# Kernel tuning notes

Hardware: AMD Instinct MI355X
Metric: run time of the kernel (lower is better)

Reference implementation:

```python
import jax, jax.numpy as jnp
import numpy as np
from jax import lax

# ---- module hyperparams (from __init__ defaults) ----
REF_TR = 2.0
NUM_BANDS = 5
FREQ_LO, FREQ_HI = 0.008, 0.12

# ---- pywt.cwt('morl') internals, precision=10 ----
NPSI = 1024                                   # 2**10 samples of the wavelet
_x = np.linspace(-8.0, 8.0, NPSI)             # morlet support [-8, 8]
STEP = float(_x[1] - _x[0])
DOMAIN = 16.0                                 # x[-1] - x[0]
_psi = np.exp(-_x ** 2 / 2.0) * np.cos(5.0 * _x)   # 'morl' wavelet psi(t)
INT_PSI = jnp.asarray(np.cumsum(_psi) * STEP, dtype=jnp.float32)  # integrate_wavelet
LMAX = 544                                    # static bound: max scale ~33.4 -> L <= 535


def _cwt_band(gpad, scale):
    """pywt conv-method CWT at one scale for all regions.
    gpad: [R, N+1+2*LMAX] = first difference of zero-extended signal, zero-padded.
    Uses identity: diff(convolve(x, K[::-1])) == correlate(diff-ext(x), K) shifted.
    """
    R = gpad.shape[0]
    N = gpad.shape[1] - 1 - 2 * LMAX
    i = jnp.arange(LMAX)
    # len(np.arange(scale*16 + 1)) for non-integer scale*16
    L0 = jnp.floor(scale * DOMAIN).astype(jnp.int32) + 2
    j = jnp.floor(i.astype(jnp.float32) / (scale * STEP)).astype(jnp.int32)
    mask = (i < L0) & (j < NPSI)              # pywt filters j < int_psi.size
    K = jnp.where(mask, INT_PSI[jnp.clip(j, 0, NPSI - 1)], 0.0)  # int_psi_scale (unreversed)
    L = mask.sum()                            # effective kernel length (mask is a prefix)
    # cross-correlation of gpad with K (lax.conv does correlation, no kernel flip)
    corr = lax.conv_general_dilated(gpad[:, None, :], K[None, None, :], (1,), 'VALID',
                                    dimension_numbers=('NCH', 'OIH', 'NCH'))[:, 0, :]
    # center crop: coef[t] = -sqrt(s) * (c[t+f+1]-c[t+f]),  f = floor((L-2)/2)
    start = LMAX + (L - 2) // 2 + 2 - L
    coef = lax.dynamic_slice(corr, (jnp.int32(0), start), (R, N))
    return jnp.abs(-jnp.sqrt(scale) * coef)


def _forward(timeseries, tr_values, log_scale_params, bandwidth_params):
    B, R, N = timeseries.shape
    tr_factors = tr_values / REF_TR
    scales = jnp.exp(log_scale_params)[None, :] / tr_factors[:, None]      # [B, bands]
    # frequency bands [B, bands, 2]
    center = 1.0 / (scales * tr_values[:, None])
    bw = bandwidth_params[None, :]
    low = jnp.maximum(FREQ_LO, center * (1.0 - bw / 2.0))
    high = jnp.minimum(FREQ_HI, center * (1.0 + bw / 2.0))
    frequency_bands = jnp.stack([low, high], axis=-1)
    # first difference of zero-extended signal: g[m] = x[m] - x[m-1], x=0 outside [0,N)
    g = jnp.diff(jnp.pad(timeseries, ((0, 0), (0, 0), (1, 1))), axis=-1)    # [B,R,N+1]
    gpad = jnp.pad(g, ((0, 0), (0, 0), (LMAX, LMAX)))
    per_sample = jax.vmap(_cwt_band, in_axes=(None, 0))                     # over bands
    coeffs = jax.vmap(per_sample, in_axes=(0, 0))(gpad, scales)             # [B,bands,R,N]
    coeffs = jnp.transpose(coeffs, (0, 2, 1, 3))                            # [B,R,bands,N]
    return coeffs, frequency_bands


def setup_inputs() -> dict:
    key = jax.random.key(0)
    k1, k2 = jax.random.split(key)
    B, R, T = 8, 400, 1200
    timeseries = jax.random.normal(k1, (B, R, T), dtype=jnp.float32)
    # realistic fMRI TRs in [1.5, 2.5] s (keeps adaptive scales <= 33.4 < LMAX/16)
    tr_values = 1.5 + jax.random.uniform(k2, (B,), dtype=jnp.float32)
    log_scale_params = jnp.linspace(np.log(5.0), np.log(25.0), NUM_BANDS).astype(jnp.float32)
    bandwidth_params = 0.1 * jnp.ones((NUM_BANDS,), dtype=jnp.float32)
    return {"timeseries": timeseries, "tr_values": tr_values,
            "log_scale_params": log_scale_params, "bandwidth_params": bandwidth_params}


def reference(timeseries, tr_values, log_scale_params, bandwidth_params):
    return _forward(timeseries, tr_values, log_scale_params, bandwidth_params)
```

## Files before the change

### kernel.cpp

```cpp
#include <hip/hip_runtime.h>
#include <math.h>

#define B_    8
#define R_    400
#define N_    1200
#define S_    5
#define LMAX_ 544
#define NPSI_ 1024
#define KPAD  560
#define WINMAX 1760
#define T_    20

#define WS_K      0
#define WS_SCALE  (40*KPAD)
#define WS_SQS    (WS_SCALE + 40)
#define WS_L      (WS_SQS + 40)
#define WS_START  (WS_L + 40)

__device__ __forceinline__ float4 lds_ld4(const float* base, int dw) {
    int g = dw >> 2;
    g ^= (g >> 3) & 7;
    return *(const float4*)(base + (g << 2));
}

__global__ __launch_bounds__(256) void setup_kernel(
    const float* __restrict__ tr,
    const float* __restrict__ lsp,
    const float* __restrict__ bwp,
    float* __restrict__ ws,
    float* __restrict__ out_bands)
{
    __shared__ double psi_sh[NPSI_];
    __shared__ float  intpsi[NPSI_];
    __shared__ double wtot[4];
    __shared__ float  scale_sh[40];
    __shared__ int    cnt_sh[40];
    const double STEP_D = 16.0 / 1023.0;
    const float  STEP_F = (float)(16.0 / 1023.0);
    const int tid = threadIdx.x;

    if (tid < 40) cnt_sh[tid] = 0;

    for (int k = tid; k < NPSI_; k += 256) {
        double x = (k == NPSI_ - 1) ? 8.0 : (-8.0 + (double)k * STEP_D);
        psi_sh[k] = exp(-x * x * 0.5) * cos(5.0 * x);
    }
    __syncthreads();

    {
        double a0 = psi_sh[4 * tid + 0], a1 = psi_sh[4 * tid + 1];
        double a2 = psi_sh[4 * tid + 2], a3 = psi_sh[4 * tid + 3];
        double s1 = a0 + a1, s2 = s1 + a2, s3 = s2 + a3;
        double run = s3;
        #pragma unroll
        for (int d = 1; d < 64; d <<= 1) {
            double o = __shfl_up(run, (unsigned)d, 64);
            if ((tid & 63) >= d) run += o;
        }
        if ((tid & 63) == 63) wtot[tid >> 6] = run;
        __syncthreads();
        double woff = 0.0;
        const int w = tid >> 6;
        #pragma unroll
        for (int k = 0; k < 4; ++k) if (k < w) woff += wtot[k];
        double excl = woff + run - s3;
        intpsi[4 * tid + 0] = (float)((excl + a0) * STEP_D);
        intpsi[4 * tid + 1] = (float)((excl + s1) * STEP_D);
        intpsi[4 * tid + 2] = (float)((excl + s2) * STEP_D);
        intpsi[4 * tid + 3] = (float)((excl + s3) * STEP_D);
    }

    if (tid < 40) {
        int b = tid / S_, s = tid % S_;
        float trf   = tr[b] / 2.0f;
        float scale = expf(lsp[s]) / trf;
        scale_sh[tid] = scale;
        ws[WS_SCALE + tid] = scale;
        ws[WS_SQS + tid]   = sqrtf(scale);
        float center = 1.0f / (scale * tr[b]);
        float bw = bwp[s];
        out_bands[2 * tid + 0] = fmaxf(0.008f, center * (1.0f - bw * 0.5f));
        out_bands[2 * tid + 1] = fminf(0.12f,  center * (1.0f + bw * 0.5f));
    }
    __syncthreads();

    {
        const int wv = tid >> 6, ln = tid & 63;
        for (int c = wv; c < 40 * 9; c += 4) {
            int p = c / 9, i = (c % 9) * 64 + ln;
            float scale = scale_sh[p];
            float sst   = scale * STEP_F;
            int   L0    = (int)floorf(scale * 16.0f) + 2;
            bool m = false;
            if (i < LMAX_) {
                int j = (int)floorf((float)i / sst);
                m = (i < L0) && (j < NPSI_);
            }
            unsigned long long bal = __ballot(m);
            if (ln == 0) atomicAdd(&cnt_sh[p], __popcll(bal));
        }
    }
    __syncthreads();
    if (tid < 40) {
        int L = cnt_sh[tid];
        ((int*)(ws + WS_L))[tid]     = L;
        ((int*)(ws + WS_START))[tid] = LMAX_ + (L - 2) / 2 + 2 - L;
    }

    for (int idx = tid; idx < 40 * KPAD; idx += 256) {
        int p = idx / KPAD, i = idx % KPAD;
        float v = 0.0f;
        if (i < LMAX_) {
            float scale = scale_sh[p];
            float sst   = scale * STEP_F;
            int   L0    = (int)floorf(scale * 16.0f) + 2;
            int   j     = (int)floorf((float)i / sst);
            if (i < L0 && j < NPSI_) {
                int jc = j < 0 ? 0 : (j > NPSI_ - 1 ? NPSI_ - 1 : j);
                v = intpsi[jc];
            }
        }
        ws[WS_K + idx] = v;
    }
}

__global__ __launch_bounds__(256) void cwt_main_kernel(
    const float* __restrict__ ts,
    const float* __restrict__ ws,
    float* __restrict__ out)
{
    const float* Kbase     = ws + WS_K;
    const float* sqs_arr   = ws + WS_SQS;
    const int*   L_arr     = (const int*)(ws + WS_L);
    const int*   start_arr = (const int*)(ws + WS_START);

    const int bid = blockIdx.x;
    const int rg  = bid % 100;
    const int b   = (bid / 100) % B_;
    const int s   = 4 - (bid / (100 * B_));
    const int pair = b * S_ + s;

    const int   L      = L_arr[pair];
    const int   start  = start_arr[pair];
    const float sqs    = sqs_arr[pair];
    const int   wstart = start - LMAX_;
    const int   Lpad   = ((L + 23) / 24) * 24;

    __shared__ __align__(16) float gwin[4 * WINMAX];

    const int tid = threadIdx.x;

    for (int wv = 0; wv < 4; ++wv) {
        const int r = rg * 4 + wv;
        const float* tsrow = ts + (size_t)(b * R_ + r) * N_;
        for (int t = tid; t < WINMAX; t += 256) {
            int k = wstart + t;
            float v = 0.0f;
            if (k >= 0 && k <= N_) {
                float a = (k < N_) ? tsrow[k]     : 0.0f;
                float c = (k > 0)  ? tsrow[k - 1] : 0.0f;
                v = a - c;
            }
            int dw = wv * WINMAX + t;
            int g  = dw >> 2;
            g ^= (g >> 3) & 7;
            gwin[(g << 2) | (dw & 3)] = v;
        }
    }
    __syncthreads();

    const int wv = tid >> 6;
    const int ln = tid & 63;
    const int t0 = T_ * (ln < 60 ? ln : 59);
    const int dwbase = wv * WINMAX + t0;
    const float* Kp = Kbase + pair * KPAD;

    float acc[T_];
    #pragma unroll
    for (int q = 0; q < T_; ++q) acc[q] = 0.0f;

    float W[24];
    #pragma unroll
    for (int m = 0; m < 5; ++m)
        *(float4*)&W[4 * m] = lds_ld4(gwin, dwbase + 4 * m);

    for (int i = 0; i < Lpad; i += 24) {
        #pragma unroll
        for (int p = 0; p < 6; ++p) {
            const int slot = (4 * p + 20) % 24;
            *(float4*)&W[slot] = lds_ld4(gwin, dwbase + i + 4 * p + 20);
            float4 k4 = *(const float4*)(Kp + i + 4 * p);
            #pragma unroll
            for (int j = 0; j < 4; ++j) {
                const float kv = (j == 0) ? k4.x : (j == 1) ? k4.y : (j == 2) ? k4.z : k4.w;
                #pragma unroll
                for (int q = 0; q < T_; ++q)
                    acc[q] = fmaf(kv, W[(4 * p + j + q) % 24], acc[q]);
            }
        }
    }

    if (ln < 60) {
        const int r = rg * 4 + wv;
        float* op = out + ((size_t)(b * R_ + r) * S_ + s) * N_ + t0;
        #pragma unroll
        for (int m = 0; m < T_ / 4; ++m) {
            float4 v;
            v.x = sqs * fabsf(acc[4 * m + 0]);
            v.y = sqs * fabsf(acc[4 * m + 1]);
            v.z = sqs * fabsf(acc[4 * m + 2]);
            v.w = sqs * fabsf(acc[4 * m + 3]);
            *(float4*)(op + 4 * m) = v;
        }
    }
}

extern "C" void kernel_launch(void* const* d_in, const int* in_sizes, int n_in,
                              void* d_out, int out_size, void* d_ws, size_t ws_size,
                              hipStream_t stream)
{
    const float* ts  = (const float*)d_in[0];
    const float* tr  = (const float*)d_in[1];
    const float* lsp = (const float*)d_in[2];
    const float* bwp = (const float*)d_in[3];
    float* out = (float*)d_out;
    float* ws  = (float*)d_ws;
    float* out_bands = out + (size_t)B_ * R_ * S_ * N_;

    hipLaunchKernelGGL(setup_kernel, dim3(1), dim3(256), 0, stream,
                       tr, lsp, bwp, ws, out_bands);
    hipLaunchKernelGGL(cwt_main_kernel, dim3(100 * B_ * S_), dim3(256), 0, stream,
                       ts, ws, out);
}
```

Before: 238.7 us.

## Restructure CWT correlation to 128-thread blocks with scalar LDS loads

```diff
diff --git a/kernel.cpp b/kernel.cpp
--- a/kernel.cpp
+++ b/kernel.cpp
@@ -8,20 +8,16 @@
 #define LMAX_ 544
 #define NPSI_ 1024
 #define KPAD  560
-#define WINMAX 1760
-#define T_    20
+#define WINMAX 1792
+#define T_    19
+#define C_    24
+#define WSZ   24
 
 #define WS_K      0
 #define WS_SCALE  (40*KPAD)
 #define WS_SQS    (WS_SCALE + 40)
-#define WS_L      (WS_SQS + 40)
-#define WS_START  (WS_L + 40)
-
-__device__ __forceinline__ float4 lds_ld4(const float* base, int dw) {
-    int g = dw >> 2;
-    g ^= (g >> 3) & 7;
-    return *(const float4*)(base + (g << 2));
-}
+#define WS_LPAD   (WS_SQS + 40)
+#define WS_WST    (WS_LPAD + 40)
 
 __global__ __launch_bounds__(256) void setup_kernel(
     const float* __restrict__ tr,
@@ -75,8 +71,7 @@
         float trf   = tr[b] / 2.0f;
         float scale = expf(lsp[s]) / trf;
         scale_sh[tid] = scale;
-        ws[WS_SCALE + tid] = scale;
-        ws[WS_SQS + tid]   = sqrtf(scale);
+        ws[WS_SQS + tid] = sqrtf(scale);
         float center = 1.0f / (scale * tr[b]);
         float bw = bwp[s];
         out_bands[2 * tid + 0] = fmaxf(0.008f, center * (1.0f - bw * 0.5f));
@@ -103,8 +98,8 @@
     __syncthreads();
     if (tid < 40) {
         int L = cnt_sh[tid];
-        ((int*)(ws + WS_L))[tid]     = L;
-        ((int*)(ws + WS_START))[tid] = LMAX_ + (L - 2) / 2 + 2 - L;
+        ((int*)(ws + WS_LPAD))[tid] = ((L + C_ - 1) / C_) * C_;
+        ((int*)(ws + WS_WST))[tid]  = (L - 2) / 2 + 2 - L;
     }
 
     for (int idx = tid; idx < 40 * KPAD; idx += 256) {
@@ -124,36 +119,33 @@
     }
 }
 
-__global__ __launch_bounds__(256) void cwt_main_kernel(
+__global__ __launch_bounds__(128) void cwt_main_kernel(
     const float* __restrict__ ts,
     const float* __restrict__ ws,
     float* __restrict__ out)
 {
-    const float* Kbase     = ws + WS_K;
-    const float* sqs_arr   = ws + WS_SQS;
-    const int*   L_arr     = (const int*)(ws + WS_L);
-    const int*   start_arr = (const int*)(ws + WS_START);
+    const float* __restrict__ Kbase = ws + WS_K;
+    const float* sqs_arr  = ws + WS_SQS;
+    const int*   Lpad_arr = (const int*)(ws + WS_LPAD);
+    const int*   wst_arr  = (const int*)(ws + WS_WST);
 
     const int bid = blockIdx.x;
-    const int rg  = bid % 100;
-    const int b   = (bid / 100) % B_;
-    const int s   = 4 - (bid / (100 * B_));
+    const int s   = 4 - bid / 1600;
+    const int rem = bid % 1600;
+    const int b   = rem / 200;
+    const int rp  = rem % 200;
     const int pair = b * S_ + s;
 
-    const int   L      = L_arr[pair];
-    const int   start  = start_arr[pair];
+    const int   Lpad   = Lpad_arr[pair];
+    const int   wstart = wst_arr[pair];
     const float sqs    = sqs_arr[pair];
-    const int   wstart = start - LMAX_;
-    const int   Lpad   = ((L + 23) / 24) * 24;
-
-    __shared__ __align__(16) float gwin[4 * WINMAX];
-
+
+    __shared__ float gwin[2][WINMAX];
     const int tid = threadIdx.x;
 
-    for (int wv = 0; wv < 4; ++wv) {
-        const int r = rg * 4 + wv;
-        const float* tsrow = ts + (size_t)(b * R_ + r) * N_;
-        for (int t = tid; t < WINMAX; t += 256) {
+    for (int rr = 0; rr < 2; ++rr) {
+        const float* tsrow = ts + (size_t)(b * R_ + rp * 2 + rr) * N_;
+        for (int t = tid; t < WINMAX; t += 128) {
             int k = wstart + t;
             float v = 0.0f;
             if (k >= 0 && k <= N_) {
@@ -161,56 +153,43 @@
                 float c = (k > 0)  ? tsrow[k - 1] : 0.0f;
                 v = a - c;
             }
-            int dw = wv * WINMAX + t;
-            int g  = dw >> 2;
-            g ^= (g >> 3) & 7;
-            gwin[(g << 2) | (dw & 3)] = v;
+            gwin[rr][t] = v;
         }
     }
     __syncthreads();
 
     const int wv = tid >> 6;
     const int ln = tid & 63;
-    const int t0 = T_ * (ln < 60 ? ln : 59);
-    const int dwbase = wv * WINMAX + t0;
-    const float* Kp = Kbase + pair * KPAD;
+    const int t0 = T_ * ln;
+    const float* gw = &gwin[wv][0];
+    const float* __restrict__ Kp = Kbase + pair * KPAD;
 
     float acc[T_];
     #pragma unroll
     for (int q = 0; q < T_; ++q) acc[q] = 0.0f;
 
-    float W[24];
+    float W[WSZ];
     #pragma unroll
-    for (int m = 0; m < 5; ++m)
-        *(float4*)&W[4 * m] = lds_ld4(gwin, dwbase + 4 * m);
-
-    for (int i = 0; i < Lpad; i += 24) {
-        #pragma unroll
-        for (int p = 0; p < 6; ++p) {
-            const int slot = (4 * p + 20) % 24;
-            *(float4*)&W[slot] = lds_ld4(gwin, dwbase + i + 4 * p + 20);
-            float4 k4 = *(const float4*)(Kp + i + 4 * p);
+    for (int x = 0; x < WSZ; ++x) W[x] = gw[t0 + x];
+
+    for (int i = 0; i < Lpad; i += C_) {
+        #pragma unroll
+        for (int u = 0; u < C_; ++u) {
+            const float kv = Kp[i + u];
             #pragma unroll
-            for (int j = 0; j < 4; ++j) {
-                const float kv = (j == 0) ? k4.x : (j == 1) ? k4.y : (j == 2) ? k4.z : k4.w;
-                #pragma unroll
-                for (int q = 0; q < T_; ++q)
-                    acc[q] = fmaf(kv, W[(4 * p + j + q) % 24], acc[q]);
-            }
-        }
-    }
-
-    if (ln < 60) {
-        const int r = rg * 4 + wv;
-        float* op = out + ((size_t)(b * R_ + r) * S_ + s) * N_ + t0;
-        #pragma unroll
-        for (int m = 0; m < T_ / 4; ++m) {
-            float4 v;
-            v.x = sqs * fabsf(acc[4 * m + 0]);
-            v.y = sqs * fabsf(acc[4 * m + 1]);
-            v.z = sqs * fabsf(acc[4 * m + 2]);
-            v.w = sqs * fabsf(acc[4 * m + 3]);
-            *(float4*)(op + 4 * m) = v;
+            for (int q = 0; q < T_; ++q)
+                acc[q] = fmaf(kv, W[(u + q) % WSZ], acc[q]);
+            W[u] = gw[t0 + i + u + WSZ];
+        }
+    }
+
+    {
+        const int r = rp * 2 + wv;
+        float* op = out + ((size_t)(b * R_ + r) * S_ + s) * N_;
+        #pragma unroll
+        for (int q = 0; q < T_; ++q) {
+            int t = t0 + q;
+            if (t < N_) op[t] = sqs * fabsf(acc[q]);
         }
     }
 }
@@ -229,6 +208,6 @@
 
     hipLaunchKernelGGL(setup_kernel, dim3(1), dim3(256), 0, stream,
                        tr, lsp, bwp, ws, out_bands);
-    hipLaunchKernelGGL(cwt_main_kernel, dim3(100 * B_ * S_), dim3(256), 0, stream,
+    hipLaunchKernelGGL(cwt_main_kernel, dim3(8000), dim3(128), 0, stream,
                        ts, ws, out);
 }
```

New measurement: 225.1 us. 5.7% less time.
